# Optimization experiments

Measured on AMD Instinct MI355X. Metric: run time of the kernel, lower is better.

The kernel has to match this reference:

```python
import jax, jax.numpy as jnp
import numpy as np

NEG = -1e9


def _siglu(x):
    return x * jax.nn.sigmoid(x)


def setup_inputs() -> dict:
    key = jax.random.key(0)
    ks = jax.random.split(key, 10)
    B, S, M, D = 2, 2048, 64, 1024
    sc = 0.02
    return {
        "tokens": jax.random.normal(ks[0], (B, S, D), jnp.float32),
        "memory": jax.random.normal(ks[1], (B, M, D), jnp.float32),
        "Wq": jax.random.normal(ks[2], (D, D), jnp.float32) * sc,
        "bq": jnp.zeros((D,), jnp.float32),
        "Wk": jax.random.normal(ks[3], (D, D), jnp.float32) * sc,
        "bk": jnp.zeros((D,), jnp.float32),
        "Wv": jax.random.normal(ks[4], (D, D), jnp.float32) * sc,
        "bv": jnp.zeros((D,), jnp.float32),
        "Wo": jax.random.normal(ks[5], (D, D), jnp.float32) * sc,
        "bo": jnp.zeros((D,), jnp.float32),
        "pool_q": jax.random.normal(ks[6], (M, D), jnp.float32),
        "cell_W": jax.random.normal(ks[7], (2 * D, 2 * D), jnp.float32) * sc,
        "cell_b": jnp.zeros((2 * D,), jnp.float32),
    }


def reference(tokens, memory, Wq, bq, Wk, bk, Wv, bv, Wo, bo, pool_q, cell_W, cell_b):
    B, S, D = tokens.shape
    M = memory.shape[1]
    H = 16
    hd = D // H
    T = M + S

    x = jnp.concatenate([memory, tokens], axis=1)  # (B, T, D)

    # combined causal mask: memory rows/cols fully visible, token block causal
    tok_mask = jnp.triu(jnp.full((S, S), NEG, jnp.float32), k=1)
    mask = jnp.zeros((T, T), jnp.float32).at[M:, M:].set(tok_mask)  # (T, T)

    def heads(w, b):
        return (x @ w.T + b).reshape(B, T, H, hd).transpose(0, 2, 1, 3)

    q = heads(Wq, bq)  # (B, H, T, hd)
    k = heads(Wk, bk)
    v = heads(Wv, bv)

    scores = jnp.einsum("bhqd,bhkd->bhqk", q, k) * (hd ** -0.5) + mask
    attn = jax.nn.softmax(scores, axis=-1)
    ctx = jnp.einsum("bhqk,bhkd->bhqd", attn, v)
    ctx = ctx.transpose(0, 2, 1, 3).reshape(B, T, D)
    attn_out = ctx @ Wo.T + bo

    x = x + attn_out  # residual
    mem_out = x[:, :M]  # (B, M, D)
    tok_out = x[:, M:]  # (B, S, D)

    # attention pooling: one learnable query per memory slot
    pscores = jnp.einsum("md,bsd->bms", pool_q, tok_out) * (D ** -0.5)
    pweights = jax.nn.softmax(pscores, axis=-1)
    summary = jnp.einsum("bms,bsd->bmd", pweights, tok_out)  # (B, M, D)

    # MinimalRNNCell (siglu-gated) applied per memory slot
    combined = jnp.concatenate([mem_out, summary], axis=-1)  # (B, M, 2D)
    update = combined @ cell_W.T + cell_b
    gate, cand = jnp.split(update, 2, axis=-1)
    gate = jax.nn.sigmoid(gate)
    new_memory = mem_out * gate + (1.0 - gate) * _siglu(cand)

    return tok_out, new_memory
```

## Files before the change

### kernel.cpp

```cpp
#include <hip/hip_runtime.h>
#include <hip/hip_bf16.h>

#define B_  2
#define S_  2048
#define M_  64
#define D_  1024
#define T_  2112
#define H_  16
#define HD_ 64
#define BT_ (B_*T_)
#define NEGBIG (-1e9f)
#define LOG2E 1.44269504f

typedef float f32x4  __attribute__((ext_vector_type(4)));
typedef short short8 __attribute__((ext_vector_type(8)));
typedef unsigned short u16x4 __attribute__((ext_vector_type(4)));
typedef __bf16 bf16x8 __attribute__((ext_vector_type(8)));

static __device__ __forceinline__ unsigned short bf16_of(float f) {
  __hip_bfloat16 h = __float2bfloat16(f);
  return __builtin_bit_cast(unsigned short, h);
}

static __device__ __forceinline__ f32x4 mfma_bf16(short8 a, short8 b, f32x4 c) {
  return __builtin_amdgcn_mfma_f32_16x16x32_bf16(
      __builtin_bit_cast(bf16x8, a), __builtin_bit_cast(bf16x8, b), c, 0, 0, 0);
}

static __device__ __forceinline__ void gload16(const void* g, void* lds) {
  __builtin_amdgcn_global_load_lds(
      (const __attribute__((address_space(1))) unsigned int*)g,
      (__attribute__((address_space(3))) unsigned int*)lds, 16, 0, 0);
}


__global__ void k_build_x(const float* __restrict__ tokens,
                          const float* __restrict__ memory,
                          unsigned short* __restrict__ xb) {
  for (int i = blockIdx.x * blockDim.x + threadIdx.x; i < BT_ * D_;
       i += gridDim.x * blockDim.x) {
    int b = i / (T_ * D_);
    int rem = i - b * (T_ * D_);
    int t = rem / D_;
    int d = rem - t * D_;
    float v = (t < M_) ? memory[((size_t)b * M_ + t) * D_ + d]
                       : tokens[((size_t)b * S_ + (t - M_)) * D_ + d];
    xb[i] = bf16_of(v);
  }
}

__global__ void k_cast_all(const float* __restrict__ Wq, const float* __restrict__ Wk,
                           const float* __restrict__ Wv, const float* __restrict__ Wo,
                           const float* __restrict__ cW, const float* __restrict__ pq,
                           unsigned short* __restrict__ Wqkvb, unsigned short* __restrict__ Wob,
                           unsigned short* __restrict__ cWb, unsigned short* __restrict__ pqb) {
  const int NW = D_ * D_;
  const int NC = 4 * D_ * D_;
  const int NP = M_ * D_;
  const int total = 4 * NW + NC + NP;
  for (int i = blockIdx.x * blockDim.x + threadIdx.x; i < total;
       i += gridDim.x * blockDim.x) {
    if (i < 3 * NW) {
      int which = i >> 20, j = i & (NW - 1);
      const float* s = (which == 0) ? Wq : (which == 1) ? Wk : Wv;
      Wqkvb[i] = bf16_of(s[j]);
    } else if (i < 4 * NW) {
      int j = i - 3 * NW;
      Wob[j] = bf16_of(Wo[j]);
    } else if (i < 4 * NW + NC) {
      int j = i - 4 * NW;
      cWb[j] = bf16_of(cW[j]);
    } else {
      int j = i - 4 * NW - NC;
      pqb[j] = bf16_of(pq[j] * 0.03125f * LOG2E);
    }
  }
}

__device__ __forceinline__ void gemm128_core(const unsigned short* __restrict__ A,
                                             const unsigned short* __restrict__ BT,
                                             int K, int m0, int n0,
                                             f32x4 acc[4][4]) {
  __shared__ __align__(16) unsigned short As[128][32];
  __shared__ __align__(16) unsigned short Bs[128][32];
  const int tid = threadIdx.x;
  const int w = tid >> 6, l = tid & 63;
  const int wr = w >> 1, wc = w & 1;
  const int srow = l >> 2;
  const int scol = (l & 3) * 8;
  f32x4 z; z[0] = z[1] = z[2] = z[3] = 0.f;
#pragma unroll
  for (int i = 0; i < 4; i++)
#pragma unroll
    for (int j = 0; j < 4; j++) acc[i][j] = z;

  for (int k0 = 0; k0 < K; k0 += 32) {
    __syncthreads();
#pragma unroll
    for (int c = 0; c < 2; c++) {
      int rbase = w * 32 + c * 16;
      gload16(&A[(size_t)(m0 + rbase + srow) * K + k0 + scol], &As[rbase][0]);
      gload16(&BT[(size_t)(n0 + rbase + srow) * K + k0 + scol], &Bs[rbase][0]);
    }
    __syncthreads();
    short8 a[4], b[4];
#pragma unroll
    for (int i = 0; i < 4; i++)
      a[i] = *(const short8*)&As[wr * 64 + i * 16 + (l & 15)][(l >> 4) * 8];
#pragma unroll
    for (int j = 0; j < 4; j++)
      b[j] = *(const short8*)&Bs[wc * 64 + j * 16 + (l & 15)][(l >> 4) * 8];
#pragma unroll
    for (int i = 0; i < 4; i++)
#pragma unroll
      for (int j = 0; j < 4; j++)
        acc[i][j] = mfma_bf16(a[i], b[j], acc[i][j]);
  }
}

__device__ __forceinline__ void gemm_core(const unsigned short* __restrict__ A,
                                          const unsigned short* __restrict__ BT,
                                          int ldk, int Klen, int m0, int n0,
                                          f32x4 acc[4]) {
  __shared__ __align__(16) unsigned short As[64][40];
  __shared__ __align__(16) unsigned short Bs[64][40];
  const int tid = threadIdx.x;
  const int w = tid >> 6, l = tid & 63;
  const int sr = tid >> 2, sc = (tid & 3) * 8;
  f32x4 z; z[0] = z[1] = z[2] = z[3] = 0.f;
  acc[0] = acc[1] = acc[2] = acc[3] = z;
  for (int k0 = 0; k0 < Klen; k0 += 32) {
    __syncthreads();
    *(short8*)&As[sr][sc] = *(const short8*)&A[(size_t)(m0 + sr) * ldk + k0 + sc];
    *(short8*)&Bs[sr][sc] = *(const short8*)&BT[(size_t)(n0 + sr) * ldk + k0 + sc];
    __syncthreads();
    short8 a = *(const short8*)&As[w * 16 + (l & 15)][(l >> 4) * 8];
#pragma unroll
    for (int n = 0; n < 4; n++) {
      short8 b = *(const short8*)&Bs[n * 16 + (l & 15)][(l >> 4) * 8];
      acc[n] = mfma_bf16(a, b, acc[n]);
    }
  }
}

__global__ __launch_bounds__(256) void k_qkv(
    const unsigned short* __restrict__ xb, const unsigned short* __restrict__ Wqkvb,
    const float* __restrict__ bq, const float* __restrict__ bk,
    const float* __restrict__ bv, unsigned short* __restrict__ qg,
    unsigned short* __restrict__ kg, unsigned short* __restrict__ vTg) {
  const int which = blockIdx.x >> 3;
  const unsigned short* W = Wqkvb + (size_t)which * D_ * D_;
  const float* bias = (which == 0) ? bq : ((which == 1) ? bk : bv);
  f32x4 acc[4][4];
  const int m0 = blockIdx.y * 128, n0 = (blockIdx.x & 7) * 128;
  gemm128_core(xb, W, D_, m0, n0, acc);
  const int tid = threadIdx.x, w = tid >> 6, l = tid & 63;
  const int wr = w >> 1, wc = w & 1;
#pragma unroll
  for (int i = 0; i < 4; i++) {
#pragma unroll
    for (int j = 0; j < 4; j++) {
#pragma unroll
      for (int r = 0; r < 4; r++) {
        int m = m0 + wr * 64 + i * 16 + (l >> 4) * 4 + r;
        int c = n0 + wc * 64 + j * 16 + (l & 15);
        int b = m / T_, t = m - b * T_;
        int h = c >> 6, dh = c & 63;
        int bh = b * H_ + h;
        float v = acc[i][j][r] + bias[c];
        if (which == 0)
          qg[((size_t)bh * T_ + t) * HD_ + dh] = bf16_of(v * 0.125f * LOG2E);
        else if (which == 1)
          kg[((size_t)bh * T_ + t) * HD_ + dh] = bf16_of(v);
        else
          vTg[((size_t)bh * HD_ + dh) * T_ + t] = bf16_of(v);
      }
    }
  }
}

__global__ __launch_bounds__(256) void k_attn(
    const unsigned short* __restrict__ qg, const unsigned short* __restrict__ kg,
    const unsigned short* __restrict__ vTg, unsigned short* __restrict__ ctx) {
  const int id = blockIdx.x;
  const int xcd = id & 7;
  const int rem = id >> 3;
  const int g = rem / 33, qtr = rem - g * 33;
  const int qt = (qtr == 0) ? 0 : 33 - qtr;
  const int bh = g * 8 + xcd;
  const int tid = threadIdx.x, w = tid >> 6, l = tid & 63;
  const int lr = l & 15, lg = l >> 4;
  __shared__ __align__(16) unsigned short Ks[2][64][64];
  __shared__ __align__(16) unsigned short Vs[2][64][64];
  __shared__ __align__(16) unsigned short Ps[4][16][72];

  const unsigned short* qb = qg + (size_t)bh * T_ * HD_;
  const unsigned short* kb = kg + (size_t)bh * T_ * HD_;
  const unsigned short* vb = vTg + (size_t)bh * HD_ * T_;

  short8 aq[2];
  const int qrow = qt * 64 + w * 16 + lr;
#pragma unroll
  for (int st = 0; st < 2; st++)
    aq[st] = *(const short8*)&qb[(size_t)qrow * HD_ + st * 32 + lg * 8];

  f32x4 zz; zz[0] = zz[1] = zz[2] = zz[3] = 0.f;
  f32x4 o[4];
  o[0] = o[1] = o[2] = o[3] = zz;
  float mrun = -1e30f, lrun = 0.f;

  const int nkt = (qt == 0) ? 33 : qt + 1;

  auto stage = [&](int buf, int kb2) {
#pragma unroll
    for (int i = 0; i < 2; i++) {
      int rr = w * 16 + i * 8 + (l >> 3);
      int swz = ((l & 7) ^ (rr & 7)) * 8;
      gload16(&kb[(size_t)(kb2 + rr) * HD_ + swz], &Ks[buf][w * 16 + i * 8][0]);
      gload16(&vb[(size_t)rr * T_ + kb2 + swz], &Vs[buf][w * 16 + i * 8][0]);
    }
  };

  stage(0, 0);
  __syncthreads();
  int cur = 0;

  for (int j = 0; j < nkt; j++) {
    const int kbase = j * 64;
    if (j + 1 < nkt) stage(cur ^ 1, kbase + 64);

    short8 bkf[2][4];
#pragma unroll
    for (int n = 0; n < 4; n++) {
      int row = n * 16 + lr;
      int sw = lr & 7;
#pragma unroll
      for (int st = 0; st < 2; st++)
        bkf[st][n] = *(const short8*)&Ks[cur][row][((st * 4 + lg) ^ sw) * 8];
    }
    f32x4 s[4];
    s[0] = s[1] = s[2] = s[3] = zz;
    __builtin_amdgcn_s_setprio(1);
#pragma unroll
    for (int st = 0; st < 2; st++)
#pragma unroll
      for (int n = 0; n < 4; n++)
        s[n] = mfma_bf16(bkf[st][n], aq[st], s[n]);
    __builtin_amdgcn_s_setprio(0);

    if (qt > 0 && j == qt) {
      const int tql = w * 16 + lr;
#pragma unroll
      for (int n = 0; n < 4; n++)
#pragma unroll
        for (int r = 0; r < 4; r++) {
          int tkl = n * 16 + lg * 4 + r;
          if (tkl > tql) s[n][r] = NEGBIG;
        }
    }
    float pm = s[0][0];
#pragma unroll
    for (int n = 0; n < 4; n++)
#pragma unroll
      for (int r = 0; r < 4; r++) pm = fmaxf(pm, s[n][r]);
    pm = fmaxf(pm, __shfl_xor(pm, 16));
    pm = fmaxf(pm, __shfl_xor(pm, 32));

    if (__any(pm > mrun + 8.f)) {
      float mn = fmaxf(mrun, pm);
      float fac = exp2f(mrun - mn);
      mrun = mn;
      lrun *= fac;
      float fr[4];
#pragma unroll
      for (int r = 0; r < 4; r++) fr[r] = __shfl(fac, lg * 4 + r);
#pragma unroll
      for (int n = 0; n < 4; n++)
#pragma unroll
        for (int r = 0; r < 4; r++) o[n][r] *= fr[r];
    }
#pragma unroll
    for (int n = 0; n < 4; n++) {
      u16x4 pk;
#pragma unroll
      for (int r = 0; r < 4; r++) {
        float p = exp2f(s[n][r] - mrun);
        lrun += p;
        pk[r] = bf16_of(p);
      }
      *(u16x4*)&Ps[w][lr][n * 16 + lg * 4] = pk;
    }

    short8 bvf[2][4];
#pragma unroll
    for (int n = 0; n < 4; n++) {
      int row = n * 16 + lr;
      int sw = lr & 7;
#pragma unroll
      for (int st = 0; st < 2; st++)
        bvf[st][n] = *(const short8*)&Vs[cur][row][((st * 4 + lg) ^ sw) * 8];
    }
    short8 ap[2];
#pragma unroll
    for (int st = 0; st < 2; st++)
      ap[st] = *(const short8*)&Ps[w][lr][st * 32 + lg * 8];
    __builtin_amdgcn_s_setprio(1);
#pragma unroll
    for (int st = 0; st < 2; st++)
#pragma unroll
      for (int n = 0; n < 4; n++)
        o[n] = mfma_bf16(ap[st], bvf[st][n], o[n]);
    __builtin_amdgcn_s_setprio(0);

    __syncthreads();
    cur ^= 1;
  }
  lrun += __shfl_xor(lrun, 16);
  lrun += __shfl_xor(lrun, 32);
  float linv[4];
#pragma unroll
  for (int r = 0; r < 4; r++) linv[r] = 1.f / __shfl(lrun, lg * 4 + r);

  const int b = bh >> 4, h = bh & 15;
#pragma unroll
  for (int n = 0; n < 4; n++)
#pragma unroll
    for (int r = 0; r < 4; r++) {
      int tq = qt * 64 + w * 16 + lg * 4 + r;
      float val = o[n][r] * linv[r];
      ctx[((size_t)(b * T_ + tq)) * D_ + h * HD_ + n * 16 + lr] = bf16_of(val);
    }
}

__global__ __launch_bounds__(256) void k_out(
    const unsigned short* __restrict__ ctxb, const unsigned short* __restrict__ Wob,
    const float* __restrict__ bo, const float* __restrict__ tokens,
    const float* __restrict__ memory, float* __restrict__ out_tok,
    unsigned short* __restrict__ tokb, unsigned short* __restrict__ tokTb,
    float* __restrict__ memout, unsigned short* __restrict__ comb) {
  f32x4 acc[4][4];
  const int m0 = blockIdx.y * 128, n0 = blockIdx.x * 128;
  gemm128_core(ctxb, Wob, D_, m0, n0, acc);
  const int tid = threadIdx.x, w = tid >> 6, l = tid & 63;
  const int wr = w >> 1, wc = w & 1;
#pragma unroll
  for (int i = 0; i < 4; i++) {
#pragma unroll
    for (int j = 0; j < 4; j++) {
#pragma unroll
      for (int r = 0; r < 4; r++) {
        int m = m0 + wr * 64 + i * 16 + (l >> 4) * 4 + r;
        int c = n0 + wc * 64 + j * 16 + (l & 15);
        int b = m / T_, t = m - b * T_;
        float xo = (t < M_) ? memory[((size_t)b * M_ + t) * D_ + c]
                            : tokens[((size_t)b * S_ + (t - M_)) * D_ + c];
        float val = acc[i][j][r] + bo[c] + xo;
        if (t < M_) {
          memout[((size_t)b * M_ + t) * D_ + c] = val;
          comb[((size_t)b * M_ + t) * (2 * D_) + c] = bf16_of(val);
        } else {
          size_t ti = (size_t)b * S_ + (t - M_);
          out_tok[ti * D_ + c] = val;
          tokb[ti * D_ + c] = bf16_of(val);
          tokTb[((size_t)b * D_ + c) * S_ + (t - M_)] = bf16_of(val);
        }
      }
    }
  }
}

__global__ __launch_bounds__(256) void k_pscore_part(
    const unsigned short* __restrict__ pqb, const unsigned short* __restrict__ tokb,
    float* __restrict__ pscp) {
  const int stile = blockIdx.x, ks = blockIdx.y, b = blockIdx.z;
  f32x4 acc[4];
  gemm_core(pqb + ks * 256, tokb + (size_t)b * S_ * D_ + ks * 256, D_, 256,
            0, stile * 64, acc);
  const int tid = threadIdx.x, w = tid >> 6, l = tid & 63;
  float* dst = pscp + ((size_t)(ks * B_ + b) * M_) * S_;
#pragma unroll
  for (int n = 0; n < 4; n++) {
#pragma unroll
    for (int r = 0; r < 4; r++) {
      int m = w * 16 + (l >> 4) * 4 + r;
      int s = stile * 64 + n * 16 + (l & 15);
      dst[(size_t)m * S_ + s] = acc[n][r];
    }
  }
}

__global__ __launch_bounds__(256) void k_psoftmax(const float* __restrict__ pscp,
                                                  unsigned short* __restrict__ pw) {
  const int row = blockIdx.x;
  const int b = row >> 6, m = row & 63;
  const int tid = threadIdx.x;
  float v[8];
  float mx = -1e30f;
#pragma unroll
  for (int i = 0; i < 8; i++) {
    int s = tid + i * 256;
    float acc = 0.f;
#pragma unroll
    for (int ks = 0; ks < 4; ks++)
      acc += pscp[((size_t)(ks * B_ + b) * M_ + m) * S_ + s];
    v[i] = acc;
    mx = fmaxf(mx, acc);
  }
#pragma unroll
  for (int off = 1; off < 64; off <<= 1) mx = fmaxf(mx, __shfl_xor(mx, off));
  __shared__ float rm[4], rs[4];
  if ((tid & 63) == 0) rm[tid >> 6] = mx;
  __syncthreads();
  mx = fmaxf(fmaxf(rm[0], rm[1]), fmaxf(rm[2], rm[3]));
  float sum = 0.f;
#pragma unroll
  for (int i = 0; i < 8; i++) {
    v[i] = exp2f(v[i] - mx);
    sum += v[i];
  }
#pragma unroll
  for (int off = 1; off < 64; off <<= 1) sum += __shfl_xor(sum, off);
  if ((tid & 63) == 0) rs[tid >> 6] = sum;
  __syncthreads();
  float inv = 1.f / (rs[0] + rs[1] + rs[2] + rs[3]);
#pragma unroll
  for (int i = 0; i < 8; i++)
    pw[(size_t)row * S_ + tid + i * 256] = bf16_of(v[i] * inv);
}

__global__ __launch_bounds__(256) void k_summary_part(
    const unsigned short* __restrict__ pw, const unsigned short* __restrict__ tokTb,
    float* __restrict__ sump) {
  const int nt = blockIdx.x, ks = blockIdx.y, b = blockIdx.z;
  f32x4 acc[4];
  gemm_core(pw + (size_t)b * M_ * S_ + ks * 256,
            tokTb + (size_t)b * D_ * S_ + ks * 256, S_, 256, 0, nt * 64, acc);
  const int tid = threadIdx.x, w = tid >> 6, l = tid & 63;
  float* dst = sump + ((size_t)(ks * B_ + b) * M_) * D_;
#pragma unroll
  for (int n = 0; n < 4; n++) {
#pragma unroll
    for (int r = 0; r < 4; r++) {
      int m = w * 16 + (l >> 4) * 4 + r;
      int c = nt * 64 + n * 16 + (l & 15);
      dst[(size_t)m * D_ + c] = acc[n][r];
    }
  }
}

__global__ void k_sumcomb(const float* __restrict__ sump,
                          unsigned short* __restrict__ comb) {
  int i = blockIdx.x * blockDim.x + threadIdx.x;
  if (i >= B_ * M_ * D_) return;
  int bm = i >> 10, c = i & 1023;
  int b = bm >> 6, m = bm & 63;
  float acc = 0.f;
#pragma unroll
  for (int ks = 0; ks < 8; ks++)
    acc += sump[((size_t)(ks * B_ + b) * M_ + m) * D_ + c];
  comb[((size_t)b * M_ + m) * (2 * D_) + D_ + c] = bf16_of(acc);
}

__global__ __launch_bounds__(256) void k_cell_part(
    const unsigned short* __restrict__ comb, const unsigned short* __restrict__ cWb,
    float* __restrict__ cellp) {
  const int nt = blockIdx.x, mt = blockIdx.y, ks = blockIdx.z;
  f32x4 acc[4];
  gemm_core(comb + ks * 512, cWb + ks * 512, 2 * D_, 512, mt * 64, nt * 64, acc);
  const int tid = threadIdx.x, w = tid >> 6, l = tid & 63;
#pragma unroll
  for (int n = 0; n < 4; n++) {
#pragma unroll
    for (int r = 0; r < 4; r++) {
      int m = mt * 64 + w * 16 + (l >> 4) * 4 + r;
      int c = nt * 64 + n * 16 + (l & 15);
      cellp[((size_t)ks * (B_ * M_) + m) * (2 * D_) + c] = acc[n][r];
    }
  }
}

__global__ void k_newmem(const float* __restrict__ cellp,
                         const float* __restrict__ cb,
                         const float* __restrict__ memout,
                         float* __restrict__ out2) {
  int i = blockIdx.x * blockDim.x + threadIdx.x;
  if (i >= B_ * M_ * D_) return;
  int r = i >> 10, d = i & 1023;
  float gsum = cb[d], csum = cb[D_ + d];
#pragma unroll
  for (int ks = 0; ks < 4; ks++) {
    gsum += cellp[((size_t)ks * (B_ * M_) + r) * (2 * D_) + d];
    csum += cellp[((size_t)ks * (B_ * M_) + r) * (2 * D_) + D_ + d];
  }
  float sg = 1.f / (1.f + __expf(-gsum));
  float sc = 1.f / (1.f + __expf(-csum));
  out2[i] = memout[i] * sg + (1.f - sg) * (csum * sc);
}

extern "C" void kernel_launch(void* const* d_in, const int* in_sizes, int n_in,
                              void* d_out, int out_size, void* d_ws, size_t ws_size,
                              hipStream_t stream) {
  const float* tokens = (const float*)d_in[0];
  const float* memory = (const float*)d_in[1];
  const float* Wq = (const float*)d_in[2];
  const float* bq = (const float*)d_in[3];
  const float* Wk = (const float*)d_in[4];
  const float* bk = (const float*)d_in[5];
  const float* Wv = (const float*)d_in[6];
  const float* bv = (const float*)d_in[7];
  const float* Wo = (const float*)d_in[8];
  const float* bo = (const float*)d_in[9];
  const float* pool_q = (const float*)d_in[10];
  const float* cell_W = (const float*)d_in[11];
  const float* cell_b = (const float*)d_in[12];

  size_t off = 0;
  auto alloc = [&](size_t bytes) -> void* {
    void* p = (char*)d_ws + off;
    off += (bytes + 255) & ~(size_t)255;
    return p;
  };
  unsigned short* xb    = (unsigned short*)alloc((size_t)BT_ * D_ * 2);
  unsigned short* Wqkvb = (unsigned short*)alloc((size_t)3 * D_ * D_ * 2);
  unsigned short* Wob   = (unsigned short*)alloc((size_t)D_ * D_ * 2);
  unsigned short* cWb   = (unsigned short*)alloc((size_t)(2 * D_) * (2 * D_) * 2);
  unsigned short* pqb   = (unsigned short*)alloc((size_t)M_ * D_ * 2);
  unsigned short* qg    = (unsigned short*)alloc((size_t)B_ * H_ * T_ * HD_ * 2);
  unsigned short* kg    = (unsigned short*)alloc((size_t)B_ * H_ * T_ * HD_ * 2);
  unsigned short* vTg   = (unsigned short*)alloc((size_t)B_ * H_ * HD_ * T_ * 2);
  unsigned short* ctxb  = (unsigned short*)alloc((size_t)BT_ * D_ * 2);
  unsigned short* tokb  = (unsigned short*)alloc((size_t)B_ * S_ * D_ * 2);
  unsigned short* tokTb = (unsigned short*)alloc((size_t)B_ * D_ * S_ * 2);
  float*          memout= (float*)alloc((size_t)B_ * M_ * D_ * 4);
  unsigned short* comb  = (unsigned short*)alloc((size_t)B_ * M_ * 2 * D_ * 2);
  unsigned short* pwt   = (unsigned short*)alloc((size_t)B_ * M_ * S_ * 2);
  float*          pscp  = (float*)alloc((size_t)4 * B_ * M_ * S_ * 4);
  float*          sump  = (float*)alloc((size_t)8 * B_ * M_ * D_ * 4);
  float*          cellp = (float*)alloc((size_t)4 * B_ * M_ * 2 * D_ * 4);

  float* out_tok = (float*)d_out;
  float* out_mem = out_tok + (size_t)B_ * S_ * D_;

  k_build_x<<<2048, 256, 0, stream>>>(tokens, memory, xb);
  k_cast_all<<<4096, 256, 0, stream>>>(Wq, Wk, Wv, Wo, cell_W, pool_q,
                                       Wqkvb, Wob, cWb, pqb);

  k_qkv<<<dim3(24, 33), 256, 0, stream>>>(xb, Wqkvb, bq, bk, bv, qg, kg, vTg);
  k_attn<<<1056, 256, 0, stream>>>(qg, kg, vTg, ctxb);
  k_out<<<dim3(8, 33), 256, 0, stream>>>(ctxb, Wob, bo, tokens, memory, out_tok,
                                         tokb, tokTb, memout, comb);
  k_pscore_part<<<dim3(32, 4, 2), 256, 0, stream>>>(pqb, tokb, pscp);
  k_psoftmax<<<B_ * M_, 256, 0, stream>>>(pscp, pwt);
  k_summary_part<<<dim3(16, 8, 2), 256, 0, stream>>>(pwt, tokTb, sump);
  k_sumcomb<<<512, 256, 0, stream>>>(sump, comb);
  k_cell_part<<<dim3(32, 2, 4), 256, 0, stream>>>(comb, cWb, cellp);
  k_newmem<<<512, 256, 0, stream>>>(cellp, cell_b, memout, out_mem);
}
```

Baseline: 219.5 us.

## Double-buffer 128x128 GEMM core with K=64 tiles and XOR-swizzled LDS

The 128x128 bf16 MFMA GEMM core now uses two LDS buffers and widens the K tile from 32 to 64. The next tile's global-to-LDS loads are issued before the MFMAs on the current tile, and one barrier per iteration replaces two. LDS columns are XOR-swizzled by row to avoid bank conflicts on the short8 fragment reads, and wave priority is raised around the MFMA block. This doubles LDS use to 64 KB per block, which may reduce occupancy, and assumes K is a multiple of 64.

```diff
diff --git a/kernel.cpp b/kernel.cpp
--- a/kernel.cpp
+++ b/kernel.cpp
@@ -81,40 +81,65 @@
                                              const unsigned short* __restrict__ BT,
                                              int K, int m0, int n0,
                                              f32x4 acc[4][4]) {
-  __shared__ __align__(16) unsigned short As[128][32];
-  __shared__ __align__(16) unsigned short Bs[128][32];
+  __shared__ __align__(16) unsigned short As[2][128][64];
+  __shared__ __align__(16) unsigned short Bs[2][128][64];
   const int tid = threadIdx.x;
   const int w = tid >> 6, l = tid & 63;
   const int wr = w >> 1, wc = w & 1;
-  const int srow = l >> 2;
-  const int scol = (l & 3) * 8;
+  const int lr = l & 15, lg = l >> 4;
   f32x4 z; z[0] = z[1] = z[2] = z[3] = 0.f;
 #pragma unroll
   for (int i = 0; i < 4; i++)
 #pragma unroll
     for (int j = 0; j < 4; j++) acc[i][j] = z;
 
-  for (int k0 = 0; k0 < K; k0 += 32) {
+  auto stage = [&](int buf, int k0) {
+#pragma unroll
+    for (int c = 0; c < 4; c++) {
+      int rbase = c * 32 + w * 8;
+      int rr = rbase + (l >> 3);
+      int u = (l & 7) ^ (rr & 7);
+      gload16(&A[(size_t)(m0 + rr) * K + k0 + u * 8], &As[buf][rbase][0]);
+      gload16(&BT[(size_t)(n0 + rr) * K + k0 + u * 8], &Bs[buf][rbase][0]);
+    }
+  };
+
+  stage(0, 0);
+  __syncthreads();
+  int cur = 0;
+  const int NK = K >> 6;
+  for (int kt = 0; kt < NK; kt++) {
+    if (kt + 1 < NK) stage(cur ^ 1, (kt + 1) << 6);
+
+    short8 a[4][2], b[4][2];
+#pragma unroll
+    for (int i = 0; i < 4; i++) {
+      int row = wr * 64 + i * 16 + lr;
+      int sw = row & 7;
+#pragma unroll
+      for (int kk = 0; kk < 2; kk++)
+        a[i][kk] = *(const short8*)&As[cur][row][(((kk << 2) | lg) ^ sw) * 8];
+    }
+#pragma unroll
+    for (int j = 0; j < 4; j++) {
+      int row = wc * 64 + j * 16 + lr;
+      int sw = row & 7;
+#pragma unroll
+      for (int kk = 0; kk < 2; kk++)
+        b[j][kk] = *(const short8*)&Bs[cur][row][(((kk << 2) | lg) ^ sw) * 8];
+    }
+    __builtin_amdgcn_s_setprio(1);
+#pragma unroll
+    for (int kk = 0; kk < 2; kk++)
+#pragma unroll
+      for (int i = 0; i < 4; i++)
+#pragma unroll
+        for (int j = 0; j < 4; j++)
+          acc[i][j] = mfma_bf16(a[i][kk], b[j][kk], acc[i][j]);
+    __builtin_amdgcn_s_setprio(0);
+
     __syncthreads();
-#pragma unroll
-    for (int c = 0; c < 2; c++) {
-      int rbase = w * 32 + c * 16;
-      gload16(&A[(size_t)(m0 + rbase + srow) * K + k0 + scol], &As[rbase][0]);
-      gload16(&BT[(size_t)(n0 + rbase + srow) * K + k0 + scol], &Bs[rbase][0]);
-    }
-    __syncthreads();
-    short8 a[4], b[4];
-#pragma unroll
-    for (int i = 0; i < 4; i++)
-      a[i] = *(const short8*)&As[wr * 64 + i * 16 + (l & 15)][(l >> 4) * 8];
-#pragma unroll
-    for (int j = 0; j < 4; j++)
-      b[j] = *(const short8*)&Bs[wc * 64 + j * 16 + (l & 15)][(l >> 4) * 8];
-#pragma unroll
-    for (int i = 0; i < 4; i++)
-#pragma unroll
-      for (int j = 0; j < 4; j++)
-        acc[i][j] = mfma_bf16(a[i], b[j], acc[i][j]);
+    cur ^= 1;
   }
 }
 
```

Result: no change. 218.4 us (-0.5%).
